# Kernel tuning notes

Measured on AMD Instinct MI355X. Metric: run time of the kernel, lower is better.

The kernel has to match this reference:

```python
import jax, jax.numpy as jnp
import numpy as np

VOCAB = 128
HIDDEN = 256


def setup_inputs() -> dict:
    key = jax.random.key(0)
    ks = jax.random.split(key, 8)
    B, S = 64, 2048
    # first feature channel: event-type ids stored as floats (module does .long())
    ev = jax.random.randint(ks[0], (B, S, 1), 0, VOCAB).astype(jnp.float32)
    num = jax.random.normal(ks[1], (B, S, 7), dtype=jnp.float32)
    X = jnp.concatenate([ev, num], axis=-1)  # [B,S,8]
    emb_table = jax.random.normal(ks[2], (VOCAB, 124), dtype=jnp.float32) * 0.1
    W_num = jax.random.normal(ks[3], (4, 7), dtype=jnp.float32) * 0.3
    b_num = jnp.zeros((4,), dtype=jnp.float32)
    W_conv = jax.random.normal(ks[4], (3 * HIDDEN, 128), dtype=jnp.float32) * 0.08
    b_conv = jnp.zeros((3 * HIDDEN,), dtype=jnp.float32)
    W_out = jax.random.normal(ks[5], (1, HIDDEN), dtype=jnp.float32) * 0.06
    b_out = jnp.zeros((1,), dtype=jnp.float32)
    return {"X": X, "emb_table": emb_table, "W_num": W_num, "b_num": b_num,
            "W_conv": W_conv, "b_conv": b_conv, "W_out": W_out, "b_out": b_out}


def reference(X, emb_table, W_num, b_num, W_conv, b_conv, W_out, b_out):
    # X: [B,S,8] -- channel 0 = event id, channels 1: = numeric attrs
    event = jax.lax.stop_gradient(X[:, :, 0]).astype(jnp.int32)   # [B,S]
    numeric = X[:, :, 1:]                                          # [B,S,7]
    emb = emb_table[event]                                         # [B,S,124]
    tn = numeric @ W_num.T + b_num                                 # [B,S,4]
    comb = jnp.concatenate([emb, tn], axis=-1)                     # [B,S,128]
    # Conv1d with kernel_size=1 == pointwise linear to 3*hidden gates
    gates = comb @ W_conv.T + b_conv                               # [B,S,3H]
    gates = jnp.transpose(gates, (1, 0, 2))                        # [S,B,3H]
    Z, F, O = jnp.split(gates, 3, axis=2)
    Z = jnp.tanh(Z)
    F = jax.nn.sigmoid(F)
    O = jax.nn.sigmoid(O)

    def step(h, zfo):
        z, f, o = zfo
        h = f * h + (1.0 - f) * z
        return h, o * h

    h0 = jnp.zeros(Z.shape[1:], dtype=Z.dtype)                     # [B,H]
    _, hs = jax.lax.scan(step, h0, (Z, F, O))                      # hs: [S,B,H]
    final_rep = hs[-1]                                             # [B,H]
    # dropout is identity at inference (dropout=0 / eval)
    return final_rep @ W_out.T + b_out                             # [B,1]
```

## Files before the change

### kernel.cpp

```cpp
#include <hip/hip_runtime.h>


typedef float f32x2 __attribute__((ext_vector_type(2)));
typedef float f32x4 __attribute__((ext_vector_type(4)));

#define NB 64
#define NS 2048
#define NH 256
#define CHUNKS 32
#define STEPS (NS / CHUNKS)
#define LOG2E 1.4426950408889634f
#define PAD 129

__global__ __launch_bounds__(256) void precompute_kernel(
    const float* __restrict__ X,
    const float* __restrict__ emb,
    const float* __restrict__ Wn,
    const float* __restrict__ bn,
    const float* __restrict__ Wc,
    const float* __restrict__ bc,
    f32x2* __restrict__ G2,
    float* __restrict__ Go,
    f32x2* __restrict__ Wg4,
    float* __restrict__ Wgo4,
    float* __restrict__ Xp)
{
    const int tid = threadIdx.x;
    const int blk = blockIdx.x;

    if (blk < 256) {
        __shared__ float M[124 * PAD];
        __shared__ float P[3][2][128];
        {
            const int e = tid >> 1, half = tid & 1;
            const f32x4* er4 = (const f32x4*)(emb + (size_t)e * 124);
            #pragma unroll
            for (int i = 0; i < 16; ++i) {
                const int idx = half * 16 + i;
                if (idx < 31) {
                    const f32x4 v = er4[idx];
                    const int k0 = idx * 4;
                    M[(k0 + 0) * PAD + e] = v.x;
                    M[(k0 + 1) * PAD + e] = v.y;
                    M[(k0 + 2) * PAD + e] = v.z;
                    M[(k0 + 3) * PAD + e] = v.w;
                }
            }
        }
        __syncthreads();

        const int e = tid & 127;
        const int h = tid >> 7;
        const int j = blk;
        const int k0 = h * 62;

        const float* __restrict__ wzr = Wc + (size_t)j * 128;
        const float* __restrict__ wfr = Wc + (size_t)(j + 256) * 128;
        const float* __restrict__ wor = Wc + (size_t)(j + 512) * 128;

        float az = 0.f, af = 0.f, ao = 0.f;
        #pragma unroll 31
        for (int i = 0; i < 62; ++i) {
            const int k = k0 + i;
            const float mv = M[k * PAD + e];
            az = fmaf(wzr[k], mv, az);
            af = fmaf(wfr[k], mv, af);
            ao = fmaf(wor[k], mv, ao);
        }
        P[0][h][e] = az; P[1][h][e] = af; P[2][h][e] = ao;
        __syncthreads();

        if (h == 0) {
            float sz = P[0][0][e] + P[0][1][e] + bc[j];
            float sf = P[1][0][e] + P[1][1][e] + bc[j + 256];
            float so = P[2][0][e] + P[2][1][e] + bc[j + 512];
            #pragma unroll
            for (int m = 0; m < 4; ++m) {
                const float bm = bn[m];
                sz = fmaf(wzr[124 + m], bm, sz);
                sf = fmaf(wfr[124 + m], bm, sf);
                so = fmaf(wor[124 + m], bm, so);
            }
            G2[(size_t)e * NH + j] = (f32x2){sz * (-2.0f * LOG2E), sf * (-LOG2E)};
            Go[(size_t)e * NH + j] = so * (-LOG2E);
        }
    } else if (blk == 256) {
        const int j = tid;
        #pragma unroll
        for (int m = 0; m < 4; ++m) {
            const float wz = Wc[(size_t)j * 128 + 124 + m];
            const float wf = Wc[(size_t)(j + 256) * 128 + 124 + m];
            const float wo = Wc[(size_t)(j + 512) * 128 + 124 + m];
            Wg4[m * NH + j]  = (f32x2){wz * (-2.0f * LOG2E), wf * (-LOG2E)};
            Wgo4[m * NH + j] = wo * (-LOG2E);
        }
    } else {
        const f32x4* X4 = (const f32x4*)X;
        f32x4* Xp4 = (f32x4*)Xp;
        float wn[4][7];
        #pragma unroll
        for (int m = 0; m < 4; ++m)
            #pragma unroll
            for (int n = 0; n < 7; ++n) wn[m][n] = Wn[m * 7 + n];

        const int base = (blk - 257) * 1024 + tid;
        #pragma unroll
        for (int u = 0; u < 4; ++u) {
            const int idx = base + u * 256;
            const f32x4 xa = X4[(size_t)idx * 2];
            const f32x4 xb = X4[(size_t)idx * 2 + 1];
            const int eo = ((int)xa.x) << 11;
            const float xs[7] = {xa.y, xa.z, xa.w, xb.x, xb.y, xb.z, xb.w};
            float y[4];
            #pragma unroll
            for (int m = 0; m < 4; ++m) {
                float s = 0.0f;
                #pragma unroll
                for (int n = 0; n < 7; ++n) s = fmaf(wn[m][n], xs[n], s);
                y[m] = s;
            }
            Xp4[(size_t)idx * 2]     = (f32x4){__int_as_float(eo), y[0], y[1], y[2]};
            Xp4[(size_t)idx * 2 + 1] = (f32x4){y[3], 0.f, 0.f, 0.f};
        }
    }
}

__global__ __launch_bounds__(256) void scan_kernel(
    const float* __restrict__ Xp,
    const f32x2* __restrict__ G2,
    const float* __restrict__ Go,
    const f32x2* __restrict__ Wg4,
    const float* __restrict__ Wgo4,
    float* __restrict__ AB,
    float* __restrict__ Olast)
{
    const int b = blockIdx.x;
    const int c = blockIdx.y;
    const int j = threadIdx.x;

    const f32x4* __restrict__ xq =
        (const f32x4*)(Xp + ((size_t)b * NS + (size_t)c * STEPS) * 8);
    const char* __restrict__ g2b = (const char*)G2;
    const int j8 = j * 8;

    const f32x2 w0 = Wg4[0 * NH + j];
    const f32x2 w1 = Wg4[1 * NH + j];
    const f32x2 w2 = Wg4[2 * NH + j];
    const f32x2 w3 = Wg4[3 * NH + j];

    float A = 1.0f, Bv = 0.0f;
    #pragma unroll
    for (int t = 0; t < STEPS; ++t) {
        const f32x4 ra = xq[2 * t];
        const float y3 = xq[2 * t + 1].x;
        f32x2 g = *(const f32x2*)(g2b + (size_t)(unsigned)__float_as_int(ra.x) + j8);
        g = __builtin_elementwise_fma(w0, (f32x2){ra.y, ra.y}, g);
        g = __builtin_elementwise_fma(w1, (f32x2){ra.z, ra.z}, g);
        g = __builtin_elementwise_fma(w2, (f32x2){ra.w, ra.w}, g);
        g = __builtin_elementwise_fma(w3, (f32x2){y3, y3}, g);

        const float ez = __builtin_amdgcn_exp2f(g.x);
        const float ef = __builtin_amdgcn_exp2f(g.y);
        const float az = 1.0f + ez, af = 1.0f + ef;
        const float r = __builtin_amdgcn_rcpf(az * af);
        const float f = r * az;
        const float z = fmaf(2.0f, r * af, -1.0f);

        A *= f;
        Bv = fmaf(f, Bv - z, z);
    }

    AB[(((size_t)c * NB + b) * 2 + 0) * NH + j] = A;
    AB[(((size_t)c * NB + b) * 2 + 1) * NH + j] = Bv;

    if (c == CHUNKS - 1) {
        const f32x4 la = xq[2 * (STEPS - 1)];
        const float ly3 = xq[2 * (STEPS - 1) + 1].x;
        const int eo = __float_as_int(la.x);
        float go = *(const float*)((const char*)Go + ((size_t)(unsigned)eo >> 1) + j * 4);
        go = fmaf(Wgo4[0 * NH + j], la.y, go);
        go = fmaf(Wgo4[1 * NH + j], la.z, go);
        go = fmaf(Wgo4[2 * NH + j], la.w, go);
        go = fmaf(Wgo4[3 * NH + j], ly3, go);
        Olast[b * NH + j] = __builtin_amdgcn_rcpf(1.0f + __builtin_amdgcn_exp2f(go));
    }
}

__global__ __launch_bounds__(256) void combine_kernel(
    const float* __restrict__ AB,
    const float* __restrict__ Olast,
    const float* __restrict__ Wout,
    const float* __restrict__ bout,
    float* __restrict__ out)
{
    const int b = blockIdx.x;
    const int j = threadIdx.x;

    float h = 0.0f;
    #pragma unroll 8
    for (int c = 0; c < CHUNKS; ++c) {
        const float A  = AB[(((size_t)c * NB + b) * 2 + 0) * NH + j];
        const float Bv = AB[(((size_t)c * NB + b) * 2 + 1) * NH + j];
        h = fmaf(A, h, Bv);
    }
    float v = Olast[b * NH + j] * h * Wout[j];

    #pragma unroll
    for (int off = 32; off > 0; off >>= 1) v += __shfl_down(v, off);
    __shared__ float red[4];
    if ((j & 63) == 0) red[j >> 6] = v;
    __syncthreads();
    if (j == 0) out[b] = red[0] + red[1] + red[2] + red[3] + bout[0];
}

extern "C" void kernel_launch(void* const* d_in, const int* in_sizes, int n_in,
                              void* d_out, int out_size, void* d_ws, size_t ws_size,
                              hipStream_t stream) {
    const float* X    = (const float*)d_in[0];
    const float* emb  = (const float*)d_in[1];
    const float* Wn   = (const float*)d_in[2];
    const float* bn   = (const float*)d_in[3];
    const float* Wc   = (const float*)d_in[4];
    const float* bc   = (const float*)d_in[5];
    const float* Wout = (const float*)d_in[6];
    const float* bout = (const float*)d_in[7];
    float* out = (float*)d_out;

    f32x2* G2   = (f32x2*)d_ws;
    float* Go   = (float*)(G2 + 128 * NH);
    f32x2* Wg4  = (f32x2*)(Go + 128 * NH);
    float* Wgo4 = (float*)(Wg4 + 4 * NH);
    float* AB   = Wgo4 + 4 * NH;
    float* Ol   = AB + (size_t)CHUNKS * NB * 2 * NH;
    float* Xp   = Ol + NB * NH;

    precompute_kernel<<<385, 256, 0, stream>>>(X, emb, Wn, bn, Wc, bc,
                                               G2, Go, Wg4, Wgo4, Xp);
    dim3 grid(NB, CHUNKS);
    scan_kernel<<<grid, 256, 0, stream>>>(Xp, G2, Go, Wg4, Wgo4, AB, Ol);
    combine_kernel<<<NB, 256, 0, stream>>>(AB, Ol, Wout, bout, out);
}
```

Measured before the change: 40.20 us.

## Stage fp16 gate table in LDS and restructure scan blocks over hidden halves

The precomputed embedding-gate table is stored as fp16 pairs, and each 1024-thread scan block copies its 128-column half into 64KB of shared memory. Per-step gathers then hit LDS instead of global/L2, and each block covers 8 (batch,chunk) slices for one hidden half. The cost is lower precision in the gate pre-activations and a one-time table copy per block. LDS use also limits occupancy to about one or two blocks per CU.

```diff
diff --git a/kernel.cpp b/kernel.cpp
--- a/kernel.cpp
+++ b/kernel.cpp
@@ -1,8 +1,9 @@
 #include <hip/hip_runtime.h>
 
 
-typedef float f32x2 __attribute__((ext_vector_type(2)));
-typedef float f32x4 __attribute__((ext_vector_type(4)));
+typedef float    f32x2 __attribute__((ext_vector_type(2)));
+typedef float    f32x4 __attribute__((ext_vector_type(4)));
+typedef _Float16 f16x2 __attribute__((ext_vector_type(2)));
 
 #define NB 64
 #define NS 2048
@@ -11,6 +12,7 @@
 #define STEPS (NS / CHUNKS)
 #define LOG2E 1.4426950408889634f
 #define PAD 129
+#define JH 128
 
 __global__ __launch_bounds__(256) void precompute_kernel(
     const float* __restrict__ X,
@@ -19,7 +21,7 @@
     const float* __restrict__ bn,
     const float* __restrict__ Wc,
     const float* __restrict__ bc,
-    f32x2* __restrict__ G2,
+    f16x2* __restrict__ G2h,
     float* __restrict__ Go,
     f32x2* __restrict__ Wg4,
     float* __restrict__ Wgo4,
@@ -81,7 +83,8 @@
                 sf = fmaf(wfr[124 + m], bm, sf);
                 so = fmaf(wor[124 + m], bm, so);
             }
-            G2[(size_t)e * NH + j] = (f32x2){sz * (-2.0f * LOG2E), sf * (-LOG2E)};
+            G2h[(size_t)e * NH + j] = (f16x2){(_Float16)(sz * (-2.0f * LOG2E)),
+                                              (_Float16)(sf * (-LOG2E))};
             Go[(size_t)e * NH + j] = so * (-LOG2E);
         }
     } else if (blk == 256) {
@@ -109,7 +112,7 @@
             const int idx = base + u * 256;
             const f32x4 xa = X4[(size_t)idx * 2];
             const f32x4 xb = X4[(size_t)idx * 2 + 1];
-            const int eo = ((int)xa.x) << 11;
+            const int eo = ((int)xa.x) << 10;
             const float xs[7] = {xa.y, xa.z, xa.w, xb.x, xb.y, xb.z, xb.w};
             float y[4];
             #pragma unroll
@@ -125,23 +128,41 @@
     }
 }
 
-__global__ __launch_bounds__(256) void scan_kernel(
+__global__ __launch_bounds__(1024) void scan_kernel(
     const float* __restrict__ Xp,
-    const f32x2* __restrict__ G2,
+    const f16x2* __restrict__ G2h,
     const float* __restrict__ Go,
     const f32x2* __restrict__ Wg4,
     const float* __restrict__ Wgo4,
     float* __restrict__ AB,
     float* __restrict__ Olast)
 {
-    const int b = blockIdx.x;
-    const int c = blockIdx.y;
-    const int j = threadIdx.x;
+    __shared__ f16x2 T[128 * JH];
+
+    const int tid = threadIdx.x;
+    const int jbase = blockIdx.y * JH;
+
+    {
+        const uint4* __restrict__ src = (const uint4*)G2h;
+        uint4* dst = (uint4*)T;
+        const int colbase = jbase >> 2;
+        #pragma unroll
+        for (int i = tid; i < 4096; i += 1024) {
+            const int e = i >> 5, c16 = i & 31;
+            dst[i] = src[e * 64 + colbase + c16];
+        }
+    }
+    __syncthreads();
+
+    const int slice = tid >> 7;
+    const int jj = tid & (JH - 1);
+    const int widx = __builtin_amdgcn_readfirstlane((int)blockIdx.x * 8 + slice);
+    const int b = widx >> 5;
+    const int c = widx & (CHUNKS - 1);
+    const int j = jbase + jj;
 
     const f32x4* __restrict__ xq =
         (const f32x4*)(Xp + ((size_t)b * NS + (size_t)c * STEPS) * 8);
-    const char* __restrict__ g2b = (const char*)G2;
-    const int j8 = j * 8;
 
     const f32x2 w0 = Wg4[0 * NH + j];
     const f32x2 w1 = Wg4[1 * NH + j];
@@ -153,7 +174,9 @@
     for (int t = 0; t < STEPS; ++t) {
         const f32x4 ra = xq[2 * t];
         const float y3 = xq[2 * t + 1].x;
-        f32x2 g = *(const f32x2*)(g2b + (size_t)(unsigned)__float_as_int(ra.x) + j8);
+        const unsigned eo = (unsigned)__float_as_int(ra.x);
+        const f16x2 gh = T[(eo >> 3) + jj];
+        f32x2 g = (f32x2){(float)gh.x, (float)gh.y};
         g = __builtin_elementwise_fma(w0, (f32x2){ra.y, ra.y}, g);
         g = __builtin_elementwise_fma(w1, (f32x2){ra.z, ra.z}, g);
         g = __builtin_elementwise_fma(w2, (f32x2){ra.w, ra.w}, g);
@@ -176,8 +199,8 @@
     if (c == CHUNKS - 1) {
         const f32x4 la = xq[2 * (STEPS - 1)];
         const float ly3 = xq[2 * (STEPS - 1) + 1].x;
-        const int eo = __float_as_int(la.x);
-        float go = *(const float*)((const char*)Go + ((size_t)(unsigned)eo >> 1) + j * 4);
+        const unsigned eo = (unsigned)__float_as_int(la.x);
+        float go = *(const float*)((const char*)Go + eo + (size_t)j * 4);
         go = fmaf(Wgo4[0 * NH + j], la.y, go);
         go = fmaf(Wgo4[1 * NH + j], la.z, go);
         go = fmaf(Wgo4[2 * NH + j], la.w, go);
@@ -226,17 +249,18 @@
     const float* bout = (const float*)d_in[7];
     float* out = (float*)d_out;
 
-    f32x2* G2   = (f32x2*)d_ws;
-    float* Go   = (float*)(G2 + 128 * NH);
-    f32x2* Wg4  = (f32x2*)(Go + 128 * NH);
-    float* Wgo4 = (float*)(Wg4 + 4 * NH);
-    float* AB   = Wgo4 + 4 * NH;
-    float* Ol   = AB + (size_t)CHUNKS * NB * 2 * NH;
-    float* Xp   = Ol + NB * NH;
+    char* w = (char*)d_ws;
+    f16x2* G2h  = (f16x2*)w;   w += 128 * NH * sizeof(f16x2);
+    float* Go   = (float*)w;   w += 128 * NH * sizeof(float);
+    f32x2* Wg4  = (f32x2*)w;   w += 4 * NH * sizeof(f32x2);
+    float* Wgo4 = (float*)w;   w += 4 * NH * sizeof(float);
+    float* AB   = (float*)w;   w += (size_t)CHUNKS * NB * 2 * NH * sizeof(float);
+    float* Ol   = (float*)w;   w += NB * NH * sizeof(float);
+    float* Xp   = (float*)w;   w += (size_t)NB * NS * 8 * sizeof(float);
 
     precompute_kernel<<<385, 256, 0, stream>>>(X, emb, Wn, bn, Wc, bc,
-                                               G2, Go, Wg4, Wgo4, Xp);
-    dim3 grid(NB, CHUNKS);
-    scan_kernel<<<grid, 256, 0, stream>>>(Xp, G2, Go, Wg4, Wgo4, AB, Ol);
+                                               G2h, Go, Wg4, Wgo4, Xp);
+    dim3 gridS(256, 2);
+    scan_kernel<<<gridS, 1024, 0, stream>>>(Xp, G2h, Go, Wg4, Wgo4, AB, Ol);
     combine_kernel<<<NB, 256, 0, stream>>>(AB, Ol, Wout, bout, out);
 }
```

After: 39.72 us. Within noise of the previous version (-1.2%).
